# Kernel tuning notes

Measured on AMD Instinct MI355X. Metric: run time of the kernel, lower is better.

The kernel has to match this reference:

```python
import jax, jax.numpy as jnp
import numpy as np

N = 100000   # nodes
E = 1600000  # edges
G = 2048     # graphs in batch
NF = 64      # node_feature_dim
D = 32       # hidden dim (hard-coded in module)
SF = 512     # solvent_feature_dim
BN_EPS = 1e-5


def setup_inputs() -> dict:
    key = jax.random.key(0)
    ks = jax.random.split(key, 24)
    s = 0.1
    return {
        "x": jax.random.normal(ks[0], (N, NF), jnp.float32),
        "edge_index": jax.random.randint(ks[1], (2, E), 0, N, dtype=jnp.int64),
        "batch": jnp.sort(jax.random.randint(ks[2], (N,), 0, G, dtype=jnp.int64)),
        "solvent_fingerprint": jax.random.uniform(ks[3], (G, SF), jnp.float32),
        # GIN layer 1 first Linear (NF->D); layers 2-5 first Linear stacked (D->D)
        "w1a": jax.random.normal(ks[4], (NF, D), jnp.float32) * s,
        "b1a": jnp.zeros((D,), jnp.float32),
        "ws_a": jax.random.normal(ks[5], (4, D, D), jnp.float32) * s,
        "bs_a": jnp.zeros((4, D), jnp.float32),
        # second Linear of all 5 GIN MLPs
        "ws_b": jax.random.normal(ks[6], (5, D, D), jnp.float32) * s,
        "bs_b": jnp.zeros((5, D), jnp.float32),
        # BatchNorm affine params per layer
        "bn_g": jnp.ones((5, D), jnp.float32),
        "bn_b": jnp.zeros((5, D), jnp.float32),
        # dense head
        "fcg_w": jax.random.normal(ks[7], (D, 128), jnp.float32) * s,
        "fcg_b": jnp.zeros((128,), jnp.float32),
        "fs1_w": jax.random.normal(ks[8], (SF, 256), jnp.float32) * s,
        "fs1_b": jnp.zeros((256,), jnp.float32),
        "fs2_w": jax.random.normal(ks[9], (256, 128), jnp.float32) * s,
        "fs2_b": jnp.zeros((128,), jnp.float32),
        "fc1_w": jax.random.normal(ks[10], (256, 1024), jnp.float32) * s,
        "fc1_b": jnp.zeros((1024,), jnp.float32),
        "fc2_w": jax.random.normal(ks[11], (1024, 256), jnp.float32) * s,
        "fc2_b": jnp.zeros((256,), jnp.float32),
        "out_w": jax.random.normal(ks[12], (256, 1), jnp.float32) * s,
        "out_b": jnp.zeros((1,), jnp.float32),
    }


def _bn_relu(h, g, b):
    # BatchNorm1d training-mode math (biased batch variance), then ReLU
    mu = h.mean(axis=0)
    var = h.var(axis=0)
    return jax.nn.relu((h - mu) * jax.lax.rsqrt(var + BN_EPS) * g + b)


def reference(x, edge_index, batch, solvent_fingerprint,
              w1a, b1a, ws_a, bs_a, ws_b, bs_b, bn_g, bn_b,
              fcg_w, fcg_b, fs1_w, fs1_b, fs2_w, fs2_b,
              fc1_w, fc1_b, fc2_w, fc2_b, out_w, out_b):
    src, dst = edge_index[0], edge_index[1]

    def gin_agg(h):
        # GINConv with eps=0: (1+eps)*x_i + sum_{j->i} x_j
        return h + jax.ops.segment_sum(h[src], dst, num_segments=N)

    # layer 1 (NF -> D)
    h = gin_agg(x)
    h = jax.nn.relu(h @ w1a + b1a) @ ws_b[0] + bs_b[0]
    h = _bn_relu(h, bn_g[0], bn_b[0])
    # layers 2-5 (D -> D)
    for i in range(4):
        h = gin_agg(h)
        h = jax.nn.relu(h @ ws_a[i] + bs_a[i]) @ ws_b[i + 1] + bs_b[i + 1]
        h = _bn_relu(h, bn_g[i + 1], bn_b[i + 1])

    pooled = jax.ops.segment_sum(h, batch, num_segments=G)  # [G, D]
    gfeat = jax.nn.relu(pooled @ fcg_w + fcg_b)             # dropout inactive (eval)

    sf = solvent_fingerprint.reshape(-1, SF)
    s = jax.nn.relu(sf @ fs1_w + fs1_b)
    s = jax.nn.relu(s @ fs2_w + fs2_b)

    z = jnp.concatenate([gfeat, s], axis=1)                 # [G, 256]
    z = jax.nn.relu(z @ fc1_w + fc1_b)
    z = jax.nn.relu(z @ fc2_w + fc2_b)
    return z @ out_w + out_b                                # [G, 1]
```

## Files before the change

kernel.cpp:

```cpp
#include <hip/hip_runtime.h>
#include <hip/hip_bf16.h>

static constexpr int N_NODES = 100000;
static constexpr int N_EDGES = 1600000;
static constexpr int N_GRAPH = 2048;
static constexpr float BN_EPS_C = 1e-5f;

static constexpr int BUCK_SHIFT = 9;
static constexpr int NB_BUCK = (N_NODES + 511) >> 9;
static constexpr int PART_B = 256;
static constexpr int CHUNK = N_EDGES / PART_B;
static constexpr int NTOT = NB_BUCK * PART_B;
static constexpr int NSLOT = 8;

typedef unsigned int uint;
typedef unsigned short ushort;


__device__ inline uint pk2(float a, float b) {
    uint ua = __float_as_uint(a), ub = __float_as_uint(b);
    ua = (ua + 0x7fffu + ((ua >> 16) & 1u)) >> 16;
    ub = (ub + 0x7fffu + ((ub >> 16) & 1u)) >> 16;
    return ua | (ub << 16);
}
__device__ inline float b2f_lo(uint u) { return __uint_as_float(u << 16); }
__device__ inline float b2f_hi(uint u) { return __uint_as_float(u & 0xffff0000u); }

__device__ inline void unpack8(uint4 v, float* f) {
    f[0] = b2f_lo(v.x); f[1] = b2f_hi(v.x);
    f[2] = b2f_lo(v.y); f[3] = b2f_hi(v.y);
    f[4] = b2f_lo(v.z); f[5] = b2f_hi(v.z);
    f[6] = b2f_lo(v.w); f[7] = b2f_hi(v.w);
}


__global__ __launch_bounds__(256) void k_bcount(const int* __restrict__ dst, int* __restrict__ cnt) {
    __shared__ int h[NB_BUCK];
    int blk = blockIdx.x, tid = threadIdx.x;
    for (int i = tid; i < NB_BUCK; i += 256) h[i] = 0;
    __syncthreads();
    int base = blk * CHUNK;
    for (int e = base + tid; e < base + CHUNK; e += 256) {
        int d = __builtin_nontemporal_load(&dst[e]);
        atomicAdd(&h[d >> BUCK_SHIFT], 1);
    }
    __syncthreads();
    for (int i = tid; i < NB_BUCK; i += 256) cnt[i * PART_B + blk] = h[i];
}

__global__ __launch_bounds__(256) void k_scan_partial2(const int* __restrict__ v, int* __restrict__ part, int n) {
    __shared__ int sw[4];
    int b = blockIdx.x, tid = threadIdx.x;
    int base = b * 1024;
    int s = 0;
#pragma unroll
    for (int r = 0; r < 4; ++r) {
        int i = base + r * 256 + tid;
        if (i < n) s += v[i];
    }
#pragma unroll
    for (int off = 32; off > 0; off >>= 1) s += __shfl_down(s, off);
    if ((tid & 63) == 0) sw[tid >> 6] = s;
    __syncthreads();
    if (tid == 0) part[b] = sw[0] + sw[1] + sw[2] + sw[3];
}

__global__ __launch_bounds__(256) void k_scan_offsets2(int* __restrict__ part, int nb, int* __restrict__ bstart) {
    __shared__ int sh[256];
    int tid = threadIdx.x;
    sh[tid] = (tid < nb) ? part[tid] : 0;
    __syncthreads();
    if (tid == 0) {
        int run = 0;
        for (int i = 0; i < nb; ++i) { int v = sh[i]; sh[i] = run; run += v; }
        bstart[NB_BUCK] = run;
    }
    __syncthreads();
    if (tid < nb) part[tid] = sh[tid];
}

__global__ __launch_bounds__(256) void k_scan_final2(int* __restrict__ cnt, const int* __restrict__ part,
                                                     int* __restrict__ bstart, int n) {
    __shared__ int wsum[4];
    int b = blockIdx.x, tid = threadIdx.x;
    int lane = tid & 63, w = tid >> 6;
    int base = b * 1024 + tid * 4;
    int v[4];
#pragma unroll
    for (int r = 0; r < 4; ++r) {
        int i = base + r;
        v[r] = (i < n) ? cnt[i] : 0;
    }
    int tsum = v[0] + v[1] + v[2] + v[3];
    int inc = tsum;
#pragma unroll
    for (int off = 1; off < 64; off <<= 1) {
        int t = __shfl_up(inc, off);
        if (lane >= off) inc += t;
    }
    if (lane == 63) wsum[w] = inc;
    __syncthreads();
    int woff = 0;
    for (int ww = 0; ww < w; ++ww) woff += wsum[ww];
    int run = part[b] + woff + (inc - tsum);
#pragma unroll
    for (int r = 0; r < 4; ++r) {
        int idx = base + r;
        if (idx < n) {
            int c = v[r];
            cnt[idx] = run;
            if ((idx & (PART_B - 1)) == 0) bstart[idx / PART_B] = run;
            run += c;
        }
    }
}

__global__ __launch_bounds__(256) void k_bpart(const int* __restrict__ src, const int* __restrict__ dst,
                                               const int* __restrict__ cnt, int2* __restrict__ ebuf) {
    __shared__ int cur[NB_BUCK];
    int blk = blockIdx.x, tid = threadIdx.x;
    for (int i = tid; i < NB_BUCK; i += 256) cur[i] = cnt[i * PART_B + blk];
    __syncthreads();
    int base = blk * CHUNK;
    for (int e = base + tid; e < base + CHUNK; e += 256) {
        int d = __builtin_nontemporal_load(&dst[e]);
        int s = __builtin_nontemporal_load(&src[e]);
        int p = atomicAdd(&cur[d >> BUCK_SHIFT], 1);
        ebuf[p] = make_int2(d, s);
    }
}

__global__ __launch_bounds__(256) void k_bfine(const int2* __restrict__ ebuf, const int* __restrict__ bstart,
                                               int* __restrict__ row_ptr, int* __restrict__ row_end,
                                               int* __restrict__ ssrc) {
    __shared__ int fh[512];
    __shared__ int wsum[4];
    int b = blockIdx.x, tid = threadIdx.x;
    int n0 = b << BUCK_SHIFT;
    int e0 = bstart[b], e1 = bstart[b + 1];
    fh[tid] = 0; fh[tid + 256] = 0;
    __syncthreads();
    for (int e = e0 + tid; e < e1; e += 256)
        atomicAdd(&fh[ebuf[e].x - n0], 1);
    __syncthreads();
    int a0 = fh[2 * tid], a1 = fh[2 * tid + 1];
    int s = a0 + a1;
    int lane = tid & 63, w = tid >> 6;
    int inc = s;
#pragma unroll
    for (int off = 1; off < 64; off <<= 1) {
        int t = __shfl_up(inc, off);
        if (lane >= off) inc += t;
    }
    if (lane == 63) wsum[w] = inc;
    __syncthreads();
    int woff = 0;
    for (int ww = 0; ww < w; ++ww) woff += wsum[ww];
    int excl = woff + inc - s;
    int p0 = excl, p1 = excl + a0;
    int node0 = n0 + 2 * tid, node1 = node0 + 1;
    if (node0 < N_NODES) { row_ptr[node0] = e0 + p0; row_end[node0] = e0 + p0 + a0; }
    if (node1 < N_NODES) { row_ptr[node1] = e0 + p1; row_end[node1] = e0 + p1 + a1; }
    fh[2 * tid] = p0; fh[2 * tid + 1] = p1;
    __syncthreads();
    for (int e = e0 + tid; e < e1; e += 256) {
        int2 v = ebuf[e];
        int p = atomicAdd(&fh[v.x - n0], 1);
        ssrc[e0 + p] = v.y;
    }
}


__global__ __launch_bounds__(256) void k_gather64b(const ushort* __restrict__ xb,
                                                   const int* __restrict__ row_ptr, const int* __restrict__ row_end,
                                                   const int* __restrict__ ssrc, float* __restrict__ out) {
    int idx = blockIdx.x * 256 + threadIdx.x;
    int node = idx >> 3;
    if (node >= N_NODES) return;
    int f8 = (idx & 7) * 8;
    float acc[8];
    unpack8(*(const uint4*)(xb + (size_t)node * 64 + f8), acc);
    int e = row_ptr[node], e1 = row_end[node];
    for (; e + 2 <= e1; e += 2) {
        int s0 = ssrc[e], s1 = ssrc[e + 1];
        uint4 va = *(const uint4*)(xb + (size_t)s0 * 64 + f8);
        uint4 vb = *(const uint4*)(xb + (size_t)s1 * 64 + f8);
        float v[8];
        unpack8(va, v);
#pragma unroll
        for (int j = 0; j < 8; ++j) acc[j] += v[j];
        unpack8(vb, v);
#pragma unroll
        for (int j = 0; j < 8; ++j) acc[j] += v[j];
    }
    if (e < e1) {
        int s = ssrc[e];
        float v[8];
        unpack8(*(const uint4*)(xb + (size_t)s * 64 + f8), v);
#pragma unroll
        for (int j = 0; j < 8; ++j) acc[j] += v[j];
    }
    float* op = out + (size_t)node * 64 + f8;
    *(float4*)op = make_float4(acc[0], acc[1], acc[2], acc[3]);
    *(float4*)(op + 4) = make_float4(acc[4], acc[5], acc[6], acc[7]);
}

__global__ __launch_bounds__(256) void k_gather64(const float* __restrict__ x,
                                                  const int* __restrict__ row_ptr, const int* __restrict__ row_end,
                                                  const int* __restrict__ ssrc, float* __restrict__ out) {
    int idx = blockIdx.x * 256 + threadIdx.x;
    int node = idx >> 4;
    if (node >= N_NODES) return;
    int f = (idx & 15) * 4;
    float4 acc = *(const float4*)(x + (size_t)node * 64 + f);
    int e1 = row_end[node];
    for (int e = row_ptr[node]; e < e1; ++e) {
        int s = ssrc[e];
        float4 v = *(const float4*)(x + (size_t)s * 64 + f);
        acc.x += v.x; acc.y += v.y; acc.z += v.z; acc.w += v.w;
    }
    *(float4*)(out + (size_t)node * 64 + f) = acc;
}

__global__ __launch_bounds__(256) void k_gather_bn_b(const ushort* __restrict__ u, const float* __restrict__ stats,
                                                     const float* __restrict__ bng, const float* __restrict__ bnb,
                                                     const int* __restrict__ row_ptr, const int* __restrict__ row_end,
                                                     const int* __restrict__ ssrc, float* __restrict__ out) {
    int idx = blockIdx.x * 256 + threadIdx.x;
    int node = idx >> 2;
    if (node >= N_NODES) return;
    int f8 = (idx & 3) * 8;
    const float inv = 1.0f / (float)N_NODES;
    float sc[8], sh[8];
    {
        float s1[8] = {0,0,0,0,0,0,0,0}, s2[8] = {0,0,0,0,0,0,0,0};
        for (int s = 0; s < NSLOT; ++s) {
            const float* sp = stats + s * 64;
            float4 a = *(const float4*)(sp + f8);
            float4 b = *(const float4*)(sp + f8 + 4);
            float4 c = *(const float4*)(sp + 32 + f8);
            float4 d = *(const float4*)(sp + 36 + f8);
            s1[0] += a.x; s1[1] += a.y; s1[2] += a.z; s1[3] += a.w;
            s1[4] += b.x; s1[5] += b.y; s1[6] += b.z; s1[7] += b.w;
            s2[0] += c.x; s2[1] += c.y; s2[2] += c.z; s2[3] += c.w;
            s2[4] += d.x; s2[5] += d.y; s2[6] += d.z; s2[7] += d.w;
        }
        float g[8], b[8];
        *(float4*)g = *(const float4*)(bng + f8); *(float4*)(g + 4) = *(const float4*)(bng + f8 + 4);
        *(float4*)b = *(const float4*)(bnb + f8); *(float4*)(b + 4) = *(const float4*)(bnb + f8 + 4);
#pragma unroll
        for (int j = 0; j < 8; ++j) {
            float mu = s1[j] * inv;
            sc[j] = rsqrtf(s2[j] * inv - mu * mu + BN_EPS_C) * g[j];
            sh[j] = b[j] - mu * sc[j];
        }
    }
    float acc[8], v[8];
    unpack8(*(const uint4*)(u + (size_t)node * 32 + f8), v);
#pragma unroll
    for (int j = 0; j < 8; ++j) acc[j] = fmaxf(fmaf(v[j], sc[j], sh[j]), 0.f);
    int e = row_ptr[node], e1 = row_end[node];
    for (; e + 2 <= e1; e += 2) {
        int s0 = ssrc[e], s1 = ssrc[e + 1];
        uint4 va = *(const uint4*)(u + (size_t)s0 * 32 + f8);
        uint4 vb = *(const uint4*)(u + (size_t)s1 * 32 + f8);
        unpack8(va, v);
#pragma unroll
        for (int j = 0; j < 8; ++j) acc[j] += fmaxf(fmaf(v[j], sc[j], sh[j]), 0.f);
        unpack8(vb, v);
#pragma unroll
        for (int j = 0; j < 8; ++j) acc[j] += fmaxf(fmaf(v[j], sc[j], sh[j]), 0.f);
    }
    if (e < e1) {
        int s = ssrc[e];
        unpack8(*(const uint4*)(u + (size_t)s * 32 + f8), v);
#pragma unroll
        for (int j = 0; j < 8; ++j) acc[j] += fmaxf(fmaf(v[j], sc[j], sh[j]), 0.f);
    }
    float* op = out + (size_t)node * 32 + f8;
    *(float4*)op = make_float4(acc[0], acc[1], acc[2], acc[3]);
    *(float4*)(op + 4) = make_float4(acc[4], acc[5], acc[6], acc[7]);
}


template <int K>
__global__ __launch_bounds__(256) void k_mlp_stats(const float* __restrict__ agg,
                                                   const float* __restrict__ Wa, const float* __restrict__ ba,
                                                   const float* __restrict__ Wb, const float* __restrict__ bb,
                                                   ushort* __restrict__ u, float* __restrict__ stats) {
    __shared__ float tile[256][36];
    __shared__ float bstats[64];
    int tid = threadIdx.x;
    if (tid < 64) bstats[tid] = 0.f;
    int node = blockIdx.x * 256 + tid;
    bool active = node < N_NODES;

    float h[32];
#pragma unroll
    for (int j = 0; j < 32; ++j) h[j] = ba[j];
    if (active) {
        const float* arow = agg + (size_t)node * K;
        for (int k = 0; k < K; k += 4) {
            float4 a4 = *(const float4*)(arow + k);
            float av[4] = {a4.x, a4.y, a4.z, a4.w};
#pragma unroll
            for (int kk = 0; kk < 4; ++kk) {
                float a = av[kk];
                const float* wr = Wa + (k + kk) * 32;
#pragma unroll
                for (int j = 0; j < 32; ++j) h[j] = fmaf(a, wr[j], h[j]);
            }
        }
    }
#pragma unroll
    for (int j = 0; j < 32; ++j) h[j] = fmaxf(h[j], 0.f);

    float uu[32];
#pragma unroll
    for (int j = 0; j < 32; ++j) uu[j] = bb[j];
#pragma unroll
    for (int k = 0; k < 32; ++k) {
        float a = h[k];
        const float* wr = Wb + k * 32;
#pragma unroll
        for (int j = 0; j < 32; ++j) uu[j] = fmaf(a, wr[j], uu[j]);
    }

    if (active) {
        uint pk[16];
#pragma unroll
        for (int j = 0; j < 16; ++j) pk[j] = pk2(uu[2 * j], uu[2 * j + 1]);
        uint4* up = (uint4*)(u + (size_t)node * 32);
        up[0] = make_uint4(pk[0], pk[1], pk[2], pk[3]);
        up[1] = make_uint4(pk[4], pk[5], pk[6], pk[7]);
        up[2] = make_uint4(pk[8], pk[9], pk[10], pk[11]);
        up[3] = make_uint4(pk[12], pk[13], pk[14], pk[15]);
    } else {
#pragma unroll
        for (int j = 0; j < 32; ++j) uu[j] = 0.f;
    }

#pragma unroll
    for (int q = 0; q < 8; ++q)
        *(float4*)&tile[tid][q * 4] = make_float4(uu[q * 4], uu[q * 4 + 1], uu[q * 4 + 2], uu[q * 4 + 3]);
    __syncthreads();
    if (tid < 128) {
        int w = tid >> 5, j = tid & 31;
        int r0 = w * 64;
        float sv = 0.f, sv2 = 0.f;
        for (int r = 0; r < 64; ++r) {
            float v = tile[r0 + r][j];
            sv += v;
            sv2 = fmaf(v, v, sv2);
        }
        atomicAdd(&bstats[j], sv);
        atomicAdd(&bstats[32 + j], sv2);
    }
    __syncthreads();
    if (tid < 64) atomicAdd(&stats[(blockIdx.x & (NSLOT - 1)) * 64 + tid], bstats[tid]);
}


__global__ __launch_bounds__(256) void k_bn_pool(const ushort* __restrict__ u, const float* __restrict__ stats,
                                                 const float* __restrict__ bng, const float* __restrict__ bnb,
                                                 const int* __restrict__ batch, float* __restrict__ pooled) {
    const int CH = 128;
    int wid = (blockIdx.x * 256 + threadIdx.x) >> 6;
    int lane = threadIdx.x & 63;
    int f = lane & 31, par = lane >> 5;
    int n0 = wid * CH;
    if (n0 >= N_NODES) return;
    int n1 = n0 + CH; if (n1 > N_NODES) n1 = N_NODES;
    const float inv = 1.0f / (float)N_NODES;
    float sv = 0.f, sq = 0.f;
    for (int s = 0; s < NSLOT; ++s) { sv += stats[s * 64 + f]; sq += stats[s * 64 + 32 + f]; }
    float mu = sv * inv;
    float var = sq * inv - mu * mu;
    float sc = rsqrtf(var + BN_EPS_C) * bng[f];
    float sh = bnb[f] - mu * sc;
    float acc = 0.f;
    int curg = -1;
    for (int n = n0 + par; n < n1; n += 2) {
        int g = batch[n];
        if (g != curg) {
            if (curg >= 0) atomicAdd(&pooled[(size_t)curg * 32 + f], acc);
            acc = 0.f; curg = g;
        }
        float v = b2f_lo((uint)u[(size_t)n * 32 + f]);
        acc += fmaxf(fmaf(v, sc, sh), 0.f);
    }
    if (curg >= 0) atomicAdd(&pooled[(size_t)curg * 32 + f], acc);
}


__global__ __launch_bounds__(256) void k_cvt_bf16(const float* __restrict__ x, ushort* __restrict__ xb, int n) {
    int i = (blockIdx.x * 256 + threadIdx.x) * 8;
    if (i >= n) return;
    float4 a = *(const float4*)(x + i);
    float4 b = *(const float4*)(x + i + 4);
    *(uint4*)(xb + i) = make_uint4(pk2(a.x, a.y), pk2(a.z, a.w), pk2(b.x, b.y), pk2(b.z, b.w));
}


#define GEMM_COMPUTE_16()                                                      \
    _Pragma("unroll")                                                          \
    for (int k = 0; k < 16; ++k) {                                             \
        float4 a4 = *(const float4*)&As[k][ty * 4];                            \
        float4 b4 = *(const float4*)&Bs[k][tx * 4];                            \
        acc[0][0] = fmaf(a4.x, b4.x, acc[0][0]);                               \
        acc[0][1] = fmaf(a4.x, b4.y, acc[0][1]);                               \
        acc[0][2] = fmaf(a4.x, b4.z, acc[0][2]);                               \
        acc[0][3] = fmaf(a4.x, b4.w, acc[0][3]);                               \
        acc[1][0] = fmaf(a4.y, b4.x, acc[1][0]);                               \
        acc[1][1] = fmaf(a4.y, b4.y, acc[1][1]);                               \
        acc[1][2] = fmaf(a4.y, b4.z, acc[1][2]);                               \
        acc[1][3] = fmaf(a4.y, b4.w, acc[1][3]);                               \
        acc[2][0] = fmaf(a4.z, b4.x, acc[2][0]);                               \
        acc[2][1] = fmaf(a4.z, b4.y, acc[2][1]);                               \
        acc[2][2] = fmaf(a4.z, b4.z, acc[2][2]);                               \
        acc[2][3] = fmaf(a4.z, b4.w, acc[2][3]);                               \
        acc[3][0] = fmaf(a4.w, b4.x, acc[3][0]);                               \
        acc[3][1] = fmaf(a4.w, b4.y, acc[3][1]);                               \
        acc[3][2] = fmaf(a4.w, b4.z, acc[3][2]);                               \
        acc[3][3] = fmaf(a4.w, b4.w, acc[3][3]);                               \
    }

__global__ __launch_bounds__(256) void k_gemm_f(const float* __restrict__ A, const float* __restrict__ B,
                                                const float* __restrict__ bias, float* __restrict__ C,
                                                int Nc, int K, int ldc, int do_relu) {
    __shared__ float As[16][64];
    __shared__ float Bs[16][64];
    int tid = threadIdx.x;
    int tx = tid & 15, ty = tid >> 4;
    int bm = blockIdx.x * 64, bn = blockIdx.y * 64;
    float acc[4][4] = {{0.f}};
    int am = tid >> 2;
    int ak = (tid & 3) * 4;
    int bk = tid >> 4;
    int bn4 = (tid & 15) * 4;
    const float* Ap = A + (size_t)(bm + am) * K + ak;
    const float* Bp = B + (size_t)bk * Nc + bn + bn4;
    float4 av = *(const float4*)Ap;
    float4 bv = *(const float4*)Bp;
    for (int k0 = 0; k0 < K; k0 += 16) {
        As[ak + 0][am] = av.x;
        As[ak + 1][am] = av.y;
        As[ak + 2][am] = av.z;
        As[ak + 3][am] = av.w;
        *(float4*)&Bs[bk][bn4] = bv;
        __syncthreads();
        if (k0 + 16 < K) {
            av = *(const float4*)(Ap + k0 + 16);
            bv = *(const float4*)(Bp + (size_t)(k0 + 16) * Nc);
        }
        GEMM_COMPUTE_16()
        __syncthreads();
    }
    float4 bi = *(const float4*)(bias + bn + tx * 4);
#pragma unroll
    for (int i = 0; i < 4; ++i) {
        float4 v;
        v.x = acc[i][0] + bi.x;
        v.y = acc[i][1] + bi.y;
        v.z = acc[i][2] + bi.z;
        v.w = acc[i][3] + bi.w;
        if (do_relu) {
            v.x = fmaxf(v.x, 0.f); v.y = fmaxf(v.y, 0.f);
            v.z = fmaxf(v.z, 0.f); v.w = fmaxf(v.w, 0.f);
        }
        *(float4*)(C + (size_t)(bm + ty * 4 + i) * ldc + bn + tx * 4) = v;
    }
}

__global__ __launch_bounds__(256) void k_gemm_p(const float* __restrict__ A, const float* __restrict__ B,
                                                float* __restrict__ psum, int Nc, int Ktot, int klen) {
    __shared__ float As[16][64];
    __shared__ float Bs[16][64];
    int tid = threadIdx.x;
    int tx = tid & 15, ty = tid >> 4;
    int bm = blockIdx.x * 64, bn = blockIdx.y * 64;
    int kb = blockIdx.z * klen;
    float acc[4][4] = {{0.f}};
    int am = tid >> 2;
    int ak = (tid & 3) * 4;
    int bk = tid >> 4;
    int bn4 = (tid & 15) * 4;
    const float* Ap = A + (size_t)(bm + am) * Ktot + kb + ak;
    const float* Bp = B + (size_t)(kb + bk) * Nc + bn + bn4;
    float4 av = *(const float4*)Ap;
    float4 bv = *(const float4*)Bp;
    for (int k0 = 0; k0 < klen; k0 += 16) {
        As[ak + 0][am] = av.x;
        As[ak + 1][am] = av.y;
        As[ak + 2][am] = av.z;
        As[ak + 3][am] = av.w;
        *(float4*)&Bs[bk][bn4] = bv;
        __syncthreads();
        if (k0 + 16 < klen) {
            av = *(const float4*)(Ap + k0 + 16);
            bv = *(const float4*)(Bp + (size_t)(k0 + 16) * Nc);
        }
        GEMM_COMPUTE_16()
        __syncthreads();
    }
    float* out = psum + (size_t)blockIdx.z * N_GRAPH * Nc;
#pragma unroll
    for (int i = 0; i < 4; ++i) {
        float4 v = make_float4(acc[i][0], acc[i][1], acc[i][2], acc[i][3]);
        *(float4*)(out + (size_t)(bm + ty * 4 + i) * Nc + bn + tx * 4) = v;
    }
}

__global__ __launch_bounds__(256) void k_reduce(const float* __restrict__ psum, const float* __restrict__ bias,
                                                float* __restrict__ C, int S, int Nc, int ldc, int do_relu) {
    int idx = blockIdx.x * 256 + threadIdx.x;
    int nq = Nc >> 2;
    if (idx >= N_GRAPH * nq) return;
    int m = idx / nq;
    int j = (idx - m * nq) * 4;
    float4 s = *(const float4*)(psum + (size_t)m * Nc + j);
    for (int z = 1; z < S; ++z) {
        float4 t = *(const float4*)(psum + (size_t)z * N_GRAPH * Nc + (size_t)m * Nc + j);
        s.x += t.x; s.y += t.y; s.z += t.z; s.w += t.w;
    }
    float4 bi = *(const float4*)(bias + j);
    s.x += bi.x; s.y += bi.y; s.z += bi.z; s.w += bi.w;
    if (do_relu) {
        s.x = fmaxf(s.x, 0.f); s.y = fmaxf(s.y, 0.f);
        s.z = fmaxf(s.z, 0.f); s.w = fmaxf(s.w, 0.f);
    }
    *(float4*)(C + (size_t)m * ldc + j) = s;
}


__global__ __launch_bounds__(256) void k_out(const float* __restrict__ z2, const float* __restrict__ w,
                                             const float* __restrict__ b, float* __restrict__ out) {
    int gid = blockIdx.x * 256 + threadIdx.x;
    int g = gid >> 6;
    int lane = threadIdx.x & 63;
    if (g >= N_GRAPH) return;
    float4 a = *(const float4*)(z2 + (size_t)g * 256 + lane * 4);
    float4 wv = *(const float4*)(w + lane * 4);
    float v = a.x * wv.x + a.y * wv.y + a.z * wv.z + a.w * wv.w;
#pragma unroll
    for (int off = 32; off > 0; off >>= 1) v += __shfl_down(v, off);
    if (lane == 0) out[g] = v + b[0];
}


extern "C" void kernel_launch(void* const* d_in, const int* in_sizes, int n_in,
                              void* d_out, int out_size, void* d_ws, size_t ws_size,
                              hipStream_t stream) {
    const float* x     = (const float*)d_in[0];
    const int*   eidx  = (const int*)d_in[1];
    const int*   batch = (const int*)d_in[2];
    const float* sf    = (const float*)d_in[3];
    const float* w1a   = (const float*)d_in[4];
    const float* b1a   = (const float*)d_in[5];
    const float* ws_a  = (const float*)d_in[6];
    const float* bs_a  = (const float*)d_in[7];
    const float* ws_b  = (const float*)d_in[8];
    const float* bs_b  = (const float*)d_in[9];
    const float* bn_g  = (const float*)d_in[10];
    const float* bn_b  = (const float*)d_in[11];
    const float* fcg_w = (const float*)d_in[12];
    const float* fcg_b = (const float*)d_in[13];
    const float* fs1_w = (const float*)d_in[14];
    const float* fs1_b = (const float*)d_in[15];
    const float* fs2_w = (const float*)d_in[16];
    const float* fs2_b = (const float*)d_in[17];
    const float* fc1_w = (const float*)d_in[18];
    const float* fc1_b = (const float*)d_in[19];
    const float* fc2_w = (const float*)d_in[20];
    const float* fc2_b = (const float*)d_in[21];
    const float* out_w = (const float*)d_in[22];
    const float* out_b = (const float*)d_in[23];
    float* dout = (float*)d_out;

    char* p = (char*)d_ws;
    float*  agg     = (float*)p;  p += (size_t)N_NODES * 64 * 4;
    ushort* ubuf    = (ushort*)p; p += (size_t)N_NODES * 32 * 2;
    int*    ssrc    = (int*)p;    p += (size_t)N_EDGES * 4;
    int*    row_ptr = (int*)p;    p += (size_t)N_NODES * 4;
    int*    row_end = (int*)p;    p += (size_t)N_NODES * 4;
    int*    cnt     = (int*)p;    p += (size_t)NTOT * 4;
    int*    part2   = (int*)p;    p += 512 * 4;
    int*    bstart  = (int*)p;    p += 256 * 4;
    float*  stats   = (float*)p;  p += (size_t)5 * NSLOT * 64 * 4;
    float*  pooled  = (float*)p;  p += (size_t)N_GRAPH * 32 * 4;
    ushort* xb      = (ushort*)p; p += (size_t)N_NODES * 64 * 2;
    bool use_xb = ((size_t)(p - (char*)d_ws) <= ws_size);

    int2* ebuf = (int2*)agg;

    float* zcat  = agg;
    float* z1buf = zcat + 2048 * 256;
    float* z2buf = z1buf + 2048 * 1024;
    float* s1buf = z2buf + 2048 * 256;
    float* psum  = s1buf + 2048 * 256;

    size_t zero_bytes = ((size_t)5 * NSLOT * 64 + (size_t)N_GRAPH * 32) * 4;
    hipMemsetAsync(stats, 0, zero_bytes, stream);

    const int* esrc = eidx;
    const int* edst = eidx + N_EDGES;

    const int scan_blocks = NTOT / 1024;
    k_bcount<<<PART_B, 256, 0, stream>>>(edst, cnt);
    k_scan_partial2<<<scan_blocks, 256, 0, stream>>>(cnt, part2, NTOT);
    k_scan_offsets2<<<1, 256, 0, stream>>>(part2, scan_blocks, bstart);
    k_scan_final2<<<scan_blocks, 256, 0, stream>>>(cnt, part2, bstart, NTOT);
    k_bpart<<<PART_B, 256, 0, stream>>>(esrc, edst, cnt, ebuf);
    k_bfine<<<NB_BUCK, 256, 0, stream>>>(ebuf, bstart, row_ptr, row_end, ssrc);

    const int mlp_blocks = (N_NODES + 255) / 256;
    const int SLOT_STRIDE = NSLOT * 64;

    if (use_xb) {
        k_cvt_bf16<<<(N_NODES * 64 / 8 + 255) / 256, 256, 0, stream>>>(x, xb, N_NODES * 64);
        k_gather64b<<<(N_NODES * 8) / 256, 256, 0, stream>>>(xb, row_ptr, row_end, ssrc, agg);
    } else {
        k_gather64<<<(N_NODES * 16) / 256, 256, 0, stream>>>(x, row_ptr, row_end, ssrc, agg);
    }
    k_mlp_stats<64><<<mlp_blocks, 256, 0, stream>>>(agg, w1a, b1a, ws_b, bs_b, ubuf, stats);
    for (int L = 1; L <= 4; ++L) {
        k_gather_bn_b<<<(N_NODES * 4 + 255) / 256, 256, 0, stream>>>(
            ubuf, stats + (size_t)(L - 1) * SLOT_STRIDE, bn_g + (L - 1) * 32, bn_b + (L - 1) * 32,
            row_ptr, row_end, ssrc, agg);
        k_mlp_stats<32><<<mlp_blocks, 256, 0, stream>>>(
            agg, ws_a + (size_t)(L - 1) * 1024, bs_a + (L - 1) * 32,
            ws_b + (size_t)L * 1024, bs_b + L * 32, ubuf, stats + (size_t)L * SLOT_STRIDE);
    }
    {
        int waves = (N_NODES + 127) / 128;
        int blocks = (waves + 3) / 4;
        k_bn_pool<<<blocks, 256, 0, stream>>>(ubuf, stats + (size_t)4 * SLOT_STRIDE,
                                              bn_g + 128, bn_b + 128, batch, pooled);
    }

    k_gemm_f<<<dim3(32, 2), 256, 0, stream>>>(pooled, fcg_w, fcg_b, zcat, 128, 32, 256, 1);
    k_gemm_p<<<dim3(32, 4, 4), 256, 0, stream>>>(sf, fs1_w, psum, 256, 512, 128);
    k_reduce<<<512, 256, 0, stream>>>(psum, fs1_b, s1buf, 4, 256, 256, 1);
    k_gemm_p<<<dim3(32, 2, 4), 256, 0, stream>>>(s1buf, fs2_w, psum, 128, 256, 64);
    k_reduce<<<256, 256, 0, stream>>>(psum, fs2_b, zcat + 128, 4, 128, 256, 1);
    k_gemm_f<<<dim3(32, 16), 256, 0, stream>>>(zcat, fc1_w, fc1_b, z1buf, 1024, 256, 1024, 1);
    k_gemm_p<<<dim3(32, 4, 4), 256, 0, stream>>>(z1buf, fc2_w, psum, 256, 1024, 256);
    k_reduce<<<512, 256, 0, stream>>>(psum, fc2_b, z2buf, 4, 256, 256, 1);
    k_out<<<512, 256, 0, stream>>>(z2buf, out_w, out_b, dout);
}
```

Baseline: 602.8 us.

## Fuse neighbor gather with GIN MLP and BN stats into one kernel per layer

Merges the gather/aggregation kernel and the MLP+BatchNorm-statistics kernel into a single kernel per GIN layer. Each node's features are split across 8 or 4 lanes, partial matvecs are reduced with cross-lane shuffles, and weights are staged in LDS. This removes the fp32 aggregation buffer round trip through global memory and halves the launch count. To avoid read/write hazards it ping-pongs between two bf16 activation buffers, at the cost of extra shuffles and redundant first-layer FLOPs per lane group.

```diff
diff --git a/kernel.cpp b/kernel.cpp
--- a/kernel.cpp
+++ b/kernel.cpp
@@ -171,71 +171,158 @@
 }
 
 
-__global__ __launch_bounds__(256) void k_gather64b(const ushort* __restrict__ xb,
-                                                   const int* __restrict__ row_ptr, const int* __restrict__ row_end,
-                                                   const int* __restrict__ ssrc, float* __restrict__ out) {
-    int idx = blockIdx.x * 256 + threadIdx.x;
+__global__ __launch_bounds__(256) void k_cvt_bf16(const float* __restrict__ x, ushort* __restrict__ xb, int n) {
+    int i = (blockIdx.x * 256 + threadIdx.x) * 8;
+    if (i >= n) return;
+    float4 a = *(const float4*)(x + i);
+    float4 b = *(const float4*)(x + i + 4);
+    *(uint4*)(xb + i) = make_uint4(pk2(a.x, a.y), pk2(a.z, a.w), pk2(b.x, b.y), pk2(b.z, b.w));
+}
+
+
+__global__ __launch_bounds__(256) void k_fused1(const ushort* __restrict__ xb,
+                                                const int* __restrict__ row_ptr, const int* __restrict__ row_end,
+                                                const int* __restrict__ ssrc,
+                                                const float* __restrict__ Wa, const float* __restrict__ ba,
+                                                const float* __restrict__ Wb, const float* __restrict__ bb,
+                                                ushort* __restrict__ uout, float* __restrict__ stats_out) {
+    __shared__ float sWa[2048];
+    __shared__ float sWb[1024];
+    __shared__ float sba[32];
+    __shared__ float sbb[32];
+    __shared__ float bstats[64];
+    int tid = threadIdx.x;
+    for (int i = tid; i < 2048; i += 256) sWa[i] = Wa[i];
+    for (int i = tid; i < 1024; i += 256) sWb[i] = Wb[i];
+    if (tid < 32) { sba[tid] = ba[tid]; sbb[tid] = bb[tid]; }
+    if (tid < 64) bstats[tid] = 0.f;
+    __syncthreads();
+
+    int idx = blockIdx.x * 256 + tid;
     int node = idx >> 3;
-    if (node >= N_NODES) return;
-    int f8 = (idx & 7) * 8;
-    float acc[8];
-    unpack8(*(const uint4*)(xb + (size_t)node * 64 + f8), acc);
-    int e = row_ptr[node], e1 = row_end[node];
-    for (; e + 2 <= e1; e += 2) {
-        int s0 = ssrc[e], s1 = ssrc[e + 1];
-        uint4 va = *(const uint4*)(xb + (size_t)s0 * 64 + f8);
-        uint4 vb = *(const uint4*)(xb + (size_t)s1 * 64 + f8);
-        float v[8];
-        unpack8(va, v);
-#pragma unroll
-        for (int j = 0; j < 8; ++j) acc[j] += v[j];
-        unpack8(vb, v);
-#pragma unroll
-        for (int j = 0; j < 8; ++j) acc[j] += v[j];
-    }
-    if (e < e1) {
-        int s = ssrc[e];
-        float v[8];
-        unpack8(*(const uint4*)(xb + (size_t)s * 64 + f8), v);
-#pragma unroll
-        for (int j = 0; j < 8; ++j) acc[j] += v[j];
-    }
-    float* op = out + (size_t)node * 64 + f8;
-    *(float4*)op = make_float4(acc[0], acc[1], acc[2], acc[3]);
-    *(float4*)(op + 4) = make_float4(acc[4], acc[5], acc[6], acc[7]);
-}
-
-__global__ __launch_bounds__(256) void k_gather64(const float* __restrict__ x,
-                                                  const int* __restrict__ row_ptr, const int* __restrict__ row_end,
-                                                  const int* __restrict__ ssrc, float* __restrict__ out) {
-    int idx = blockIdx.x * 256 + threadIdx.x;
-    int node = idx >> 4;
-    if (node >= N_NODES) return;
-    int f = (idx & 15) * 4;
-    float4 acc = *(const float4*)(x + (size_t)node * 64 + f);
-    int e1 = row_end[node];
-    for (int e = row_ptr[node]; e < e1; ++e) {
-        int s = ssrc[e];
-        float4 v = *(const float4*)(x + (size_t)s * 64 + f);
-        acc.x += v.x; acc.y += v.y; acc.z += v.z; acc.w += v.w;
-    }
-    *(float4*)(out + (size_t)node * 64 + f) = acc;
-}
-
-__global__ __launch_bounds__(256) void k_gather_bn_b(const ushort* __restrict__ u, const float* __restrict__ stats,
-                                                     const float* __restrict__ bng, const float* __restrict__ bnb,
-                                                     const int* __restrict__ row_ptr, const int* __restrict__ row_end,
-                                                     const int* __restrict__ ssrc, float* __restrict__ out) {
-    int idx = blockIdx.x * 256 + threadIdx.x;
+    int sl = idx & 7;
+    int f8 = sl * 8;
+    bool active = node < N_NODES;
+
+    float acc[8] = {0.f, 0.f, 0.f, 0.f, 0.f, 0.f, 0.f, 0.f};
+    if (active) {
+        unpack8(*(const uint4*)(xb + (size_t)node * 64 + f8), acc);
+        int e = row_ptr[node], e1 = row_end[node];
+        for (; e + 2 <= e1; e += 2) {
+            int s0 = ssrc[e], s1 = ssrc[e + 1];
+            uint4 va = *(const uint4*)(xb + (size_t)s0 * 64 + f8);
+            uint4 vb = *(const uint4*)(xb + (size_t)s1 * 64 + f8);
+            float v[8];
+            unpack8(va, v);
+#pragma unroll
+            for (int j = 0; j < 8; ++j) acc[j] += v[j];
+            unpack8(vb, v);
+#pragma unroll
+            for (int j = 0; j < 8; ++j) acc[j] += v[j];
+        }
+        if (e < e1) {
+            int s = ssrc[e];
+            float v[8];
+            unpack8(*(const uint4*)(xb + (size_t)s * 64 + f8), v);
+#pragma unroll
+            for (int j = 0; j < 8; ++j) acc[j] += v[j];
+        }
+    }
+
+    float pj[32];
+#pragma unroll
+    for (int j = 0; j < 32; ++j) pj[j] = 0.f;
+#pragma unroll
+    for (int kk = 0; kk < 8; ++kk) {
+        float a = acc[kk];
+        const float4* wr = (const float4*)(sWa + (f8 + kk) * 32);
+#pragma unroll
+        for (int j4 = 0; j4 < 8; ++j4) {
+            float4 wv = wr[j4];
+            pj[j4 * 4 + 0] = fmaf(a, wv.x, pj[j4 * 4 + 0]);
+            pj[j4 * 4 + 1] = fmaf(a, wv.y, pj[j4 * 4 + 1]);
+            pj[j4 * 4 + 2] = fmaf(a, wv.z, pj[j4 * 4 + 2]);
+            pj[j4 * 4 + 3] = fmaf(a, wv.w, pj[j4 * 4 + 3]);
+        }
+    }
+#pragma unroll
+    for (int j = 0; j < 32; ++j) {
+        pj[j] += __shfl_xor(pj[j], 1);
+        pj[j] += __shfl_xor(pj[j], 2);
+        pj[j] += __shfl_xor(pj[j], 4);
+        pj[j] = fmaxf(pj[j] + sba[j], 0.f);
+    }
+
+    int j0 = sl * 4;
+    float uu[4];
+#pragma unroll
+    for (int j = 0; j < 4; ++j) uu[j] = sbb[j0 + j];
+#pragma unroll
+    for (int k = 0; k < 32; ++k) {
+        float a = pj[k];
+        const float4* wr = (const float4*)(sWb + k * 32 + j0);
+        float4 wv = wr[0];
+        uu[0] = fmaf(a, wv.x, uu[0]);
+        uu[1] = fmaf(a, wv.y, uu[1]);
+        uu[2] = fmaf(a, wv.z, uu[2]);
+        uu[3] = fmaf(a, wv.w, uu[3]);
+    }
+
+    if (active) {
+        uint2 pkv = make_uint2(pk2(uu[0], uu[1]), pk2(uu[2], uu[3]));
+        *(uint2*)(uout + (size_t)node * 32 + j0) = pkv;
+    } else {
+#pragma unroll
+        for (int j = 0; j < 4; ++j) uu[j] = 0.f;
+    }
+
+#pragma unroll
+    for (int j = 0; j < 4; ++j) {
+        float v = uu[j];
+        float v2 = v * v;
+        v += __shfl_xor(v, 8);  v2 += __shfl_xor(v2, 8);
+        v += __shfl_xor(v, 16); v2 += __shfl_xor(v2, 16);
+        v += __shfl_xor(v, 32); v2 += __shfl_xor(v2, 32);
+        if ((tid & 63) < 8) {
+            atomicAdd(&bstats[j0 + j], v);
+            atomicAdd(&bstats[32 + j0 + j], v2);
+        }
+    }
+    __syncthreads();
+    if (tid < 64) atomicAdd(&stats_out[(blockIdx.x & (NSLOT - 1)) * 64 + tid], bstats[tid]);
+}
+
+
+__global__ __launch_bounds__(256) void k_fused(const ushort* __restrict__ uin, ushort* __restrict__ uout,
+                                               const float* __restrict__ stats_in, float* __restrict__ stats_out,
+                                               const float* __restrict__ bng, const float* __restrict__ bnb,
+                                               const int* __restrict__ row_ptr, const int* __restrict__ row_end,
+                                               const int* __restrict__ ssrc,
+                                               const float* __restrict__ Wa, const float* __restrict__ ba,
+                                               const float* __restrict__ Wb, const float* __restrict__ bb) {
+    __shared__ float sWa[1024];
+    __shared__ float sWb[1024];
+    __shared__ float sba[32];
+    __shared__ float sbb[32];
+    __shared__ float bstats[64];
+    int tid = threadIdx.x;
+    for (int i = tid; i < 1024; i += 256) { sWa[i] = Wa[i]; sWb[i] = Wb[i]; }
+    if (tid < 32) { sba[tid] = ba[tid]; sbb[tid] = bb[tid]; }
+    if (tid < 64) bstats[tid] = 0.f;
+    __syncthreads();
+
+    int idx = blockIdx.x * 256 + tid;
     int node = idx >> 2;
-    if (node >= N_NODES) return;
-    int f8 = (idx & 3) * 8;
+    int sl = idx & 3;
+    int f8 = sl * 8;
+    bool active = node < N_NODES;
+
     const float inv = 1.0f / (float)N_NODES;
     float sc[8], sh[8];
     {
         float s1[8] = {0,0,0,0,0,0,0,0}, s2[8] = {0,0,0,0,0,0,0,0};
         for (int s = 0; s < NSLOT; ++s) {
-            const float* sp = stats + s * 64;
+            const float* sp = stats_in + s * 64;
             float4 a = *(const float4*)(sp + f8);
             float4 b = *(const float4*)(sp + f8 + 4);
             float4 c = *(const float4*)(sp + 32 + f8);
@@ -255,109 +342,97 @@
             sh[j] = b[j] - mu * sc[j];
         }
     }
-    float acc[8], v[8];
-    unpack8(*(const uint4*)(u + (size_t)node * 32 + f8), v);
-#pragma unroll
-    for (int j = 0; j < 8; ++j) acc[j] = fmaxf(fmaf(v[j], sc[j], sh[j]), 0.f);
-    int e = row_ptr[node], e1 = row_end[node];
-    for (; e + 2 <= e1; e += 2) {
-        int s0 = ssrc[e], s1 = ssrc[e + 1];
-        uint4 va = *(const uint4*)(u + (size_t)s0 * 32 + f8);
-        uint4 vb = *(const uint4*)(u + (size_t)s1 * 32 + f8);
-        unpack8(va, v);
-#pragma unroll
-        for (int j = 0; j < 8; ++j) acc[j] += fmaxf(fmaf(v[j], sc[j], sh[j]), 0.f);
-        unpack8(vb, v);
-#pragma unroll
-        for (int j = 0; j < 8; ++j) acc[j] += fmaxf(fmaf(v[j], sc[j], sh[j]), 0.f);
-    }
-    if (e < e1) {
-        int s = ssrc[e];
-        unpack8(*(const uint4*)(u + (size_t)s * 32 + f8), v);
-#pragma unroll
-        for (int j = 0; j < 8; ++j) acc[j] += fmaxf(fmaf(v[j], sc[j], sh[j]), 0.f);
-    }
-    float* op = out + (size_t)node * 32 + f8;
-    *(float4*)op = make_float4(acc[0], acc[1], acc[2], acc[3]);
-    *(float4*)(op + 4) = make_float4(acc[4], acc[5], acc[6], acc[7]);
-}
-
-
-template <int K>
-__global__ __launch_bounds__(256) void k_mlp_stats(const float* __restrict__ agg,
-                                                   const float* __restrict__ Wa, const float* __restrict__ ba,
-                                                   const float* __restrict__ Wb, const float* __restrict__ bb,
-                                                   ushort* __restrict__ u, float* __restrict__ stats) {
-    __shared__ float tile[256][36];
-    __shared__ float bstats[64];
-    int tid = threadIdx.x;
-    if (tid < 64) bstats[tid] = 0.f;
-    int node = blockIdx.x * 256 + tid;
-    bool active = node < N_NODES;
-
-    float h[32];
-#pragma unroll
-    for (int j = 0; j < 32; ++j) h[j] = ba[j];
+
+    float acc[8] = {0.f, 0.f, 0.f, 0.f, 0.f, 0.f, 0.f, 0.f};
     if (active) {
-        const float* arow = agg + (size_t)node * K;
-        for (int k = 0; k < K; k += 4) {
-            float4 a4 = *(const float4*)(arow + k);
-            float av[4] = {a4.x, a4.y, a4.z, a4.w};
-#pragma unroll
-            for (int kk = 0; kk < 4; ++kk) {
-                float a = av[kk];
-                const float* wr = Wa + (k + kk) * 32;
-#pragma unroll
-                for (int j = 0; j < 32; ++j) h[j] = fmaf(a, wr[j], h[j]);
-            }
-        }
-    }
-#pragma unroll
-    for (int j = 0; j < 32; ++j) h[j] = fmaxf(h[j], 0.f);
-
-    float uu[32];
-#pragma unroll
-    for (int j = 0; j < 32; ++j) uu[j] = bb[j];
+        float v[8];
+        unpack8(*(const uint4*)(uin + (size_t)node * 32 + f8), v);
+#pragma unroll
+        for (int j = 0; j < 8; ++j) acc[j] = fmaxf(fmaf(v[j], sc[j], sh[j]), 0.f);
+        int e = row_ptr[node], e1 = row_end[node];
+        for (; e + 2 <= e1; e += 2) {
+            int s0 = ssrc[e], s1 = ssrc[e + 1];
+            uint4 va = *(const uint4*)(uin + (size_t)s0 * 32 + f8);
+            uint4 vb = *(const uint4*)(uin + (size_t)s1 * 32 + f8);
+            unpack8(va, v);
+#pragma unroll
+            for (int j = 0; j < 8; ++j) acc[j] += fmaxf(fmaf(v[j], sc[j], sh[j]), 0.f);
+            unpack8(vb, v);
+#pragma unroll
+            for (int j = 0; j < 8; ++j) acc[j] += fmaxf(fmaf(v[j], sc[j], sh[j]), 0.f);
+        }
+        if (e < e1) {
+            int s = ssrc[e];
+            unpack8(*(const uint4*)(uin + (size_t)s * 32 + f8), v);
+#pragma unroll
+            for (int j = 0; j < 8; ++j) acc[j] += fmaxf(fmaf(v[j], sc[j], sh[j]), 0.f);
+        }
+    }
+
+    float pj[32];
+#pragma unroll
+    for (int j = 0; j < 32; ++j) pj[j] = 0.f;
+#pragma unroll
+    for (int kk = 0; kk < 8; ++kk) {
+        float a = acc[kk];
+        const float4* wr = (const float4*)(sWa + (f8 + kk) * 32);
+#pragma unroll
+        for (int j4 = 0; j4 < 8; ++j4) {
+            float4 wv = wr[j4];
+            pj[j4 * 4 + 0] = fmaf(a, wv.x, pj[j4 * 4 + 0]);
+            pj[j4 * 4 + 1] = fmaf(a, wv.y, pj[j4 * 4 + 1]);
+            pj[j4 * 4 + 2] = fmaf(a, wv.z, pj[j4 * 4 + 2]);
+            pj[j4 * 4 + 3] = fmaf(a, wv.w, pj[j4 * 4 + 3]);
+        }
+    }
+#pragma unroll
+    for (int j = 0; j < 32; ++j) {
+        pj[j] += __shfl_xor(pj[j], 1);
+        pj[j] += __shfl_xor(pj[j], 2);
+        pj[j] = fmaxf(pj[j] + sba[j], 0.f);
+    }
+
+    float uu[8];
+#pragma unroll
+    for (int j = 0; j < 8; ++j) uu[j] = sbb[f8 + j];
 #pragma unroll
     for (int k = 0; k < 32; ++k) {
-        float a = h[k];
-        const float* wr = Wb + k * 32;
-#pragma unroll
-        for (int j = 0; j < 32; ++j) uu[j] = fmaf(a, wr[j], uu[j]);
+        float a = pj[k];
+        const float4* wr = (const float4*)(sWb + k * 32 + f8);
+        float4 w0 = wr[0], w1 = wr[1];
+        uu[0] = fmaf(a, w0.x, uu[0]);
+        uu[1] = fmaf(a, w0.y, uu[1]);
+        uu[2] = fmaf(a, w0.z, uu[2]);
+        uu[3] = fmaf(a, w0.w, uu[3]);
+        uu[4] = fmaf(a, w1.x, uu[4]);
+        uu[5] = fmaf(a, w1.y, uu[5]);
+        uu[6] = fmaf(a, w1.z, uu[6]);
+        uu[7] = fmaf(a, w1.w, uu[7]);
     }
 
     if (active) {
-        uint pk[16];
-#pragma unroll
-        for (int j = 0; j < 16; ++j) pk[j] = pk2(uu[2 * j], uu[2 * j + 1]);
-        uint4* up = (uint4*)(u + (size_t)node * 32);
-        up[0] = make_uint4(pk[0], pk[1], pk[2], pk[3]);
-        up[1] = make_uint4(pk[4], pk[5], pk[6], pk[7]);
-        up[2] = make_uint4(pk[8], pk[9], pk[10], pk[11]);
-        up[3] = make_uint4(pk[12], pk[13], pk[14], pk[15]);
+        uint4 pkv = make_uint4(pk2(uu[0], uu[1]), pk2(uu[2], uu[3]), pk2(uu[4], uu[5]), pk2(uu[6], uu[7]));
+        *(uint4*)(uout + (size_t)node * 32 + f8) = pkv;
     } else {
 #pragma unroll
-        for (int j = 0; j < 32; ++j) uu[j] = 0.f;
-    }
-
-#pragma unroll
-    for (int q = 0; q < 8; ++q)
-        *(float4*)&tile[tid][q * 4] = make_float4(uu[q * 4], uu[q * 4 + 1], uu[q * 4 + 2], uu[q * 4 + 3]);
-    __syncthreads();
-    if (tid < 128) {
-        int w = tid >> 5, j = tid & 31;
-        int r0 = w * 64;
-        float sv = 0.f, sv2 = 0.f;
-        for (int r = 0; r < 64; ++r) {
-            float v = tile[r0 + r][j];
-            sv += v;
-            sv2 = fmaf(v, v, sv2);
-        }
-        atomicAdd(&bstats[j], sv);
-        atomicAdd(&bstats[32 + j], sv2);
-    }
-    __syncthreads();
-    if (tid < 64) atomicAdd(&stats[(blockIdx.x & (NSLOT - 1)) * 64 + tid], bstats[tid]);
+        for (int j = 0; j < 8; ++j) uu[j] = 0.f;
+    }
+
+#pragma unroll
+    for (int j = 0; j < 8; ++j) {
+        float v = uu[j];
+        float v2 = v * v;
+        v += __shfl_xor(v, 4);  v2 += __shfl_xor(v2, 4);
+        v += __shfl_xor(v, 8);  v2 += __shfl_xor(v2, 8);
+        v += __shfl_xor(v, 16); v2 += __shfl_xor(v2, 16);
+        v += __shfl_xor(v, 32); v2 += __shfl_xor(v2, 32);
+        if ((tid & 63) < 4) {
+            atomicAdd(&bstats[f8 + j], v);
+            atomicAdd(&bstats[32 + f8 + j], v2);
+        }
+    }
+    __syncthreads();
+    if (tid < 64) atomicAdd(&stats_out[(blockIdx.x & (NSLOT - 1)) * 64 + tid], bstats[tid]);
 }
 
 
@@ -390,15 +465,6 @@
         acc += fmaxf(fmaf(v, sc, sh), 0.f);
     }
     if (curg >= 0) atomicAdd(&pooled[(size_t)curg * 32 + f], acc);
-}
-
-
-__global__ __launch_bounds__(256) void k_cvt_bf16(const float* __restrict__ x, ushort* __restrict__ xb, int n) {
-    int i = (blockIdx.x * 256 + threadIdx.x) * 8;
-    if (i >= n) return;
-    float4 a = *(const float4*)(x + i);
-    float4 b = *(const float4*)(x + i + 4);
-    *(uint4*)(xb + i) = make_uint4(pk2(a.x, a.y), pk2(a.z, a.w), pk2(b.x, b.y), pk2(b.z, b.w));
 }
 
 
@@ -578,8 +644,9 @@
     float* dout = (float*)d_out;
 
     char* p = (char*)d_ws;
-    float*  agg     = (float*)p;  p += (size_t)N_NODES * 64 * 4;
-    ushort* ubuf    = (ushort*)p; p += (size_t)N_NODES * 32 * 2;
+    float*  scr     = (float*)p;  p += (size_t)N_NODES * 64 * 4;
+    ushort* u0      = (ushort*)p; p += (size_t)N_NODES * 32 * 2;
+    ushort* u1      = (ushort*)p; p += (size_t)N_NODES * 32 * 2;
     int*    ssrc    = (int*)p;    p += (size_t)N_EDGES * 4;
     int*    row_ptr = (int*)p;    p += (size_t)N_NODES * 4;
     int*    row_end = (int*)p;    p += (size_t)N_NODES * 4;
@@ -589,11 +656,10 @@
     float*  stats   = (float*)p;  p += (size_t)5 * NSLOT * 64 * 4;
     float*  pooled  = (float*)p;  p += (size_t)N_GRAPH * 32 * 4;
     ushort* xb      = (ushort*)p; p += (size_t)N_NODES * 64 * 2;
-    bool use_xb = ((size_t)(p - (char*)d_ws) <= ws_size);
-
-    int2* ebuf = (int2*)agg;
-
-    float* zcat  = agg;
+
+    int2* ebuf = (int2*)scr;
+
+    float* zcat  = scr;
     float* z1buf = zcat + 2048 * 256;
     float* z2buf = z1buf + 2048 * 1024;
     float* s1buf = z2buf + 2048 * 256;
@@ -613,28 +679,29 @@
     k_bpart<<<PART_B, 256, 0, stream>>>(esrc, edst, cnt, ebuf);
     k_bfine<<<NB_BUCK, 256, 0, stream>>>(ebuf, bstart, row_ptr, row_end, ssrc);
 
-    const int mlp_blocks = (N_NODES + 255) / 256;
     const int SLOT_STRIDE = NSLOT * 64;
 
-    if (use_xb) {
-        k_cvt_bf16<<<(N_NODES * 64 / 8 + 255) / 256, 256, 0, stream>>>(x, xb, N_NODES * 64);
-        k_gather64b<<<(N_NODES * 8) / 256, 256, 0, stream>>>(xb, row_ptr, row_end, ssrc, agg);
-    } else {
-        k_gather64<<<(N_NODES * 16) / 256, 256, 0, stream>>>(x, row_ptr, row_end, ssrc, agg);
-    }
-    k_mlp_stats<64><<<mlp_blocks, 256, 0, stream>>>(agg, w1a, b1a, ws_b, bs_b, ubuf, stats);
+    k_cvt_bf16<<<(N_NODES * 64 / 8 + 255) / 256, 256, 0, stream>>>(x, xb, N_NODES * 64);
+    k_fused1<<<(N_NODES * 8) / 256, 256, 0, stream>>>(xb, row_ptr, row_end, ssrc,
+                                                      w1a, b1a, ws_b, bs_b, u0, stats);
+
+    ushort* uin = u0;
+    ushort* uout = u1;
     for (int L = 1; L <= 4; ++L) {
-        k_gather_bn_b<<<(N_NODES * 4 + 255) / 256, 256, 0, stream>>>(
-            ubuf, stats + (size_t)(L - 1) * SLOT_STRIDE, bn_g + (L - 1) * 32, bn_b + (L - 1) * 32,
-            row_ptr, row_end, ssrc, agg);
-        k_mlp_stats<32><<<mlp_blocks, 256, 0, stream>>>(
-            agg, ws_a + (size_t)(L - 1) * 1024, bs_a + (L - 1) * 32,
-            ws_b + (size_t)L * 1024, bs_b + L * 32, ubuf, stats + (size_t)L * SLOT_STRIDE);
-    }
+        k_fused<<<(N_NODES * 4 + 255) / 256, 256, 0, stream>>>(
+            uin, uout,
+            stats + (size_t)(L - 1) * SLOT_STRIDE, stats + (size_t)L * SLOT_STRIDE,
+            bn_g + (L - 1) * 32, bn_b + (L - 1) * 32,
+            row_ptr, row_end, ssrc,
+            ws_a + (size_t)(L - 1) * 1024, bs_a + (L - 1) * 32,
+            ws_b + (size_t)L * 1024, bs_b + L * 32);
+        ushort* t = uin; uin = uout; uout = t;
+    }
+
     {
         int waves = (N_NODES + 127) / 128;
         int blocks = (waves + 3) / 4;
-        k_bn_pool<<<blocks, 256, 0, stream>>>(ubuf, stats + (size_t)4 * SLOT_STRIDE,
+        k_bn_pool<<<blocks, 256, 0, stream>>>(uin, stats + (size_t)4 * SLOT_STRIDE,
                                               bn_g + 128, bn_b + 128, batch, pooled);
     }
 
```

After: 620.3 us. 1.03x slower.
